# Kernel tuning notes

Measured on AMD Instinct MI355X. Metric: run time of the kernel, lower is better.

Reference implementation:

```python
import jax, jax.numpy as jnp
import numpy as np

CURVS = (-1.0, 0.0, 1.0, -0.5)
N, E, B = 50000, 800000, 128
IN, HID, OUT, GHID = 128, 128, 128, 32
K = len(CURVS)
TAU_MIN, TAU_MAX = 0.05, 10.0
EPS = 1e-15


def _vnorm(x):
    return jnp.maximum(jnp.linalg.norm(x, axis=-1, keepdims=True), EPS)


def tan_k(x, k):
    if k > 0:
        sk = np.sqrt(k)
        return jnp.tan(x * sk) / sk
    if k < 0:
        sk = np.sqrt(-k)
        return jnp.tanh(x * sk) / sk
    return x


def artan_k(x, k):
    if k > 0:
        sk = np.sqrt(k)
        return jnp.arctan(x * sk) / sk
    if k < 0:
        sk = np.sqrt(-k)
        return jnp.arctanh(jnp.clip(x * sk, -1.0 + 1e-7, 1.0 - 1e-7)) / sk
    return x


def project(x, k):
    # clip inside Poincare ball for k<0; identity otherwise (geoopt Stereographic.projx)
    if k < 0:
        maxn = (1.0 - 1e-5) / np.sqrt(-k)
        n = _vnorm(x)
        return jnp.where(n > maxn, x * (maxn / n), x)
    return x


def expmap0(u, k):
    n = _vnorm(u)
    return project(tan_k(n, k) * u / n, k)


def logmap0(y, k):
    n = _vnorm(y)
    return artan_k(n, k) * y / n


def mobius_add(x, y, k):
    x2 = jnp.sum(x * x, -1, keepdims=True)
    y2 = jnp.sum(y * y, -1, keepdims=True)
    xy = jnp.sum(x * y, -1, keepdims=True)
    num = (1.0 - 2.0 * k * xy - k * y2) * x + (1.0 + k * x2) * y
    den = jnp.maximum(1.0 - 2.0 * k * xy + k * k * x2 * y2, 1e-15)
    return project(num / den, k)


def mobius_matvec(W, x, k):
    mx = x @ W.T
    if k == 0:
        return mx
    xn = _vnorm(x)
    mxn = _vnorm(mx)
    res = tan_k(mxn / xn * artan_k(xn, k), k) * mx / mxn
    res = jnp.where(jnp.sum(jnp.abs(mx), -1, keepdims=True) == 0.0, 0.0, res)
    return project(res, k)


def dist(x, y, k):
    return 2.0 * artan_k(_vnorm(mobius_add(-x, y, k)), k)[..., 0]


def setup_inputs():
    key = jax.random.key(0)
    ks = jax.random.split(key, 12)
    x = jax.random.normal(ks[0], (N, IN), jnp.float32)
    edge_index = jax.random.randint(ks[1], (2, E), 0, N)
    batch = jnp.sort(jax.random.randint(ks[2], (N,), 0, B))
    s1 = float(np.sqrt(2.0 / (IN + HID)))
    s2 = float(np.sqrt(2.0 / (HID + OUT)))
    sg1 = float(np.sqrt(2.0 / (IN + GHID)))
    sg2 = float(np.sqrt(2.0 / (GHID + OUT)))
    raw0 = float(np.log(np.expm1(1.0 - TAU_MIN)))
    return {
        "x": x,
        "edge_index": edge_index,
        "batch": batch,
        "expert_w1": jax.random.normal(ks[3], (K, HID, IN), jnp.float32) * s1,
        "expert_b1": jnp.zeros((K, HID), jnp.float32),
        "expert_w2": jax.random.normal(ks[4], (K, OUT, HID), jnp.float32) * s2,
        "expert_b2": jnp.zeros((K, OUT), jnp.float32),
        "gate_w1": jax.random.normal(ks[5], (GHID, IN), jnp.float32) * sg1,
        "gate_b1": jnp.zeros((GHID,), jnp.float32),
        "gate_w2": jax.random.normal(ks[6], (OUT, GHID), jnp.float32) * sg2,
        "gate_b2": jnp.zeros((OUT,), jnp.float32),
        "gate_u": jax.random.normal(ks[7], (K, OUT), jnp.float32) * 0.02,
        "tau_raw": jnp.full((K,), raw0, jnp.float32),
    }


def _graph_norm(edge_index):
    loops = jnp.arange(N)
    row = jnp.concatenate([edge_index[0], loops])
    col = jnp.concatenate([edge_index[1], loops])
    deg = jax.ops.segment_sum(jnp.ones(E + N, jnp.float32), col, num_segments=N)
    dinv = deg ** -0.5  # deg >= 1 due to self loops
    return row, col, dinv[row] * dinv[col]


def _kappa_conv(xm, W, b, row, col, enorm, k):
    h = mobius_matvec(W, xm, k)
    bias_pt = expmap0(b[None, :], k)  # proju at origin is identity
    h = mobius_add(h, bias_pt, k)
    t = logmap0(h, k)  # [N, out]
    agg = jax.ops.segment_sum(enorm[:, None] * t[row], col, num_segments=N)
    return expmap0(agg, k)


def reference(x, edge_index, batch, expert_w1, expert_b1, expert_w2, expert_b2,
              gate_w1, gate_b1, gate_w2, gate_b2, gate_u, tau_raw):
    x = x.astype(jnp.float32)
    row, col, enorm = _graph_norm(edge_index)
    counts = jnp.maximum(
        jax.ops.segment_sum(jnp.ones(N, jnp.float32), batch, num_segments=B), 1.0)[:, None]

    # --- Riemannian experts ---
    embs = []
    for i, kv in enumerate(CURVS):
        xm = expmap0(x, kv)  # manifold init (proju at origin = identity)
        xm = _kappa_conv(xm, expert_w1[i], expert_b1[i], row, col, enorm, kv)
        xm = _kappa_conv(xm, expert_w2[i], expert_b2[i], row, col, enorm, kv)
        z = logmap0(xm, kv)
        embs.append(jax.ops.segment_sum(z, batch, num_segments=B) / counts)
    features = jnp.concatenate(embs, axis=-1)  # [B, K*OUT]

    # --- Euclidean gating encoder (GCN) ---
    def gcn(h, W, b):
        m = (h @ W.T)
        out = jax.ops.segment_sum(enorm[:, None] * m[row], col, num_segments=N) + b
        return jax.nn.relu(out)

    g = gcn(x, gate_w1, gate_b1)
    g = gcn(g, gate_w2, gate_b2)
    hgate = jax.ops.segment_sum(g, batch, num_segments=B) / counts  # [B, OUT]

    # --- Geometric distance gate ---
    tau = jnp.clip(jax.nn.softplus(tau_raw) + TAU_MIN, TAU_MIN, TAU_MAX)
    dists = []
    for i, kv in enumerate(CURVS):
        zk = expmap0(hgate, kv)
        yk = expmap0(gate_u[i][None, :], kv)
        dists.append(dist(zk, yk, kv))
    dists = jnp.stack(dists, axis=-1)  # [B, K]
    weights = jax.nn.softmax(-dists / tau[None, :], axis=-1)

    scaled = features * jnp.repeat(weights, OUT, axis=1)
    return scaled, weights, dists, tau
```

## Files before the change

kernel.cpp:

```cpp
#include <hip/hip_runtime.h>
#include <math.h>

#define NN 50000
#define EE 800000
#define ETOT (EE + NN)
#define BB 128
#define DIM 128
#define GHID 32
#define CHUNK 128
#define NCHUNK ((ETOT + CHUNK - 1) / CHUNK)
#define SCB 196

typedef _Float16 f16;
typedef _Float16 f16x2 __attribute__((ext_vector_type(2)));
typedef _Float16 f16x8 __attribute__((ext_vector_type(8)));
typedef float f32x4 __attribute__((ext_vector_type(4)));

struct CurvPack {
  float k[4], sk[4], mx[4], thr2[4];
};

__device__ __forceinline__ float wsum64(float v) {
#pragma unroll
  for (int m = 32; m; m >>= 1) v += __shfl_xor(v, m, 64);
  return v;
}

__device__ __forceinline__ float tan_k_d(float x, float kv, float sk) {
  if (kv > 0.f) return tanf(x * sk) / sk;
  if (kv < 0.f) return tanhf(x * sk) / sk;
  return x;
}

__device__ __forceinline__ float artan_k_d(float x, float kv, float sk) {
  if (kv > 0.f) return atanf(x * sk) / sk;
  if (kv < 0.f) {
    float t = x * sk;
    t = fminf(fmaxf(t, -1.f + 1e-7f), 1.f - 1e-7f);
    return atanhf(t) / sk;
  }
  return x;
}

__device__ __forceinline__ float proj_scale_d(float n, float kv, float maxn) {
  if (kv < 0.f && n > maxn) return maxn / n;
  return 1.f;
}

__global__ void k_init(float* __restrict__ deg, int n) {
  int i = blockIdx.x * 256 + threadIdx.x;
  if (i < n) deg[i] = 1.0f;
}

__global__ void k_counts(const int* __restrict__ batch, int* __restrict__ boff,
                         float* __restrict__ counts, int n) {
  int b = threadIdx.x;
  if (b <= 128) {
    int lo = 0, hi = n;
    while (lo < hi) {
      int mid = (lo + hi) >> 1;
      if (batch[mid] < b) lo = mid + 1; else hi = mid;
    }
    boff[b] = lo;
  }
  __syncthreads();
  if (b < 128) counts[b] = (float)(boff[b + 1] - boff[b]);
}

__global__ void k_deg(const int* __restrict__ ei, float* __restrict__ deg, int e) {
  int i = blockIdx.x * 256 + threadIdx.x;
  if (i < e) atomicAdd(&deg[ei[e + i]], 1.0f);
}

__global__ void k_dinv(float* __restrict__ deg, int* __restrict__ ideg, int n) {
  int i = blockIdx.x * 256 + threadIdx.x;
  if (i < n) {
    float d = deg[i];
    ideg[i] = (int)(d + 0.5f);
    deg[i] = 1.0f / sqrtf(d);
  }
}

__global__ void k_scanA(const int* __restrict__ ideg, int* __restrict__ bsum, int n) {
  __shared__ int ls[4];
  int i = blockIdx.x * 256 + threadIdx.x;
  int v = (i < n) ? ideg[i] : 0;
#pragma unroll
  for (int m = 1; m < 64; m <<= 1) v += __shfl_xor(v, m, 64);
  if ((threadIdx.x & 63) == 0) ls[threadIdx.x >> 6] = v;
  __syncthreads();
  if (threadIdx.x == 0) bsum[blockIdx.x] = ls[0] + ls[1] + ls[2] + ls[3];
}

__global__ void k_scanB(int* __restrict__ bsum, int nb) {
  __shared__ int wsh[4];
  int tid = threadIdx.x;
  int lane = tid & 63, w = tid >> 6;
  int v = (tid < nb) ? bsum[tid] : 0;
  int x = v;
#pragma unroll
  for (int o = 1; o < 64; o <<= 1) {
    int t = __shfl_up(x, o, 64);
    if (lane >= o) x += t;
  }
  if (lane == 63) wsh[w] = x;
  __syncthreads();
  int add = 0;
  for (int k2 = 0; k2 < w; k2++) add += wsh[k2];
  if (tid < nb) bsum[tid] = add + x - v;
}

__global__ void k_scanC(const int* __restrict__ ideg, const int* __restrict__ bsum,
                        int* __restrict__ off, int* __restrict__ cursor, int n) {
  __shared__ int wsh[4];
  int i = blockIdx.x * 256 + threadIdx.x;
  int lane = threadIdx.x & 63, w = threadIdx.x >> 6;
  int v = (i < n) ? ideg[i] : 0;
  int x = v;
#pragma unroll
  for (int o = 1; o < 64; o <<= 1) {
    int t = __shfl_up(x, o, 64);
    if (lane >= o) x += t;
  }
  if (lane == 63) wsh[w] = x;
  __syncthreads();
  int add = bsum[blockIdx.x];
  for (int k2 = 0; k2 < w; k2++) add += wsh[k2];
  int excl = add + x - v;
  if (i < n) {
    off[i] = excl;
    cursor[i] = excl;
  }
  if (i == n - 1) off[n] = excl + v;
}

__global__ void k_bnodes(const int* __restrict__ off, int* __restrict__ bnode, int nchunk,
                         int n) {
  int g = blockIdx.x * 256 + threadIdx.x;
  if (g >= nchunk) return;
  int e0 = g * CHUNK;
  int lo = 0, hi = n;
  while (hi - lo > 1) {
    int mid = (lo + hi) >> 1;
    if (off[mid] <= e0) lo = mid; else hi = mid;
  }
  bnode[g] = lo;
}

__global__ void k_bslot(const int* __restrict__ bnode, int* __restrict__ bslot, int nchunk) {
  int g = blockIdx.x * 256 + threadIdx.x;
  if (g >= nchunk) return;
  int v = bnode[g];
  int lo = 0, hi = g;
  while (lo < hi) {
    int mid = (lo + hi) >> 1;
    if (bnode[mid] < v) lo = mid + 1; else hi = mid;
  }
  bslot[g] = lo;
}

__device__ __forceinline__ bool span_head(const int* bnode, const int* bslot, const int* off,
                                          int g, int& nd) {
  if (bslot[g] != g) return false;
  nd = bnode[g];
  int s = off[nd], e = off[nd + 1];
  return (s / CHUNK) != ((e - 1) / CHUNK);
}

__global__ void k_zeroc(const int* __restrict__ bnode, const int* __restrict__ bslot,
                        const int* __restrict__ off, float* __restrict__ aggc, int nchunk) {
  int g = blockIdx.x * 4 + (threadIdx.x >> 6);
  int lane = threadIdx.x & 63;
  if (g >= nchunk) return;
  int nd;
  if (!span_head(bnode, bslot, off, g, nd)) return;
  float2 z = make_float2(0.f, 0.f);
#pragma unroll
  for (int i = 0; i < 5; i++) ((float2*)aggc)[(size_t)g * 320 + i * 64 + lane] = z;
}

__global__ void k_place(const int* __restrict__ ei, const float* __restrict__ dinv,
                        int* __restrict__ cursor, int2* __restrict__ esw, int e, int n) {
  int i = blockIdx.x * 256 + threadIdx.x;
  int et = e + n;
  if (i >= et) return;
  int r_, c_;
  if (i < e) {
    r_ = ei[i];
    c_ = ei[e + i];
  } else {
    r_ = i - e;
    c_ = i - e;
  }
  int p = atomicAdd(&cursor[c_], 1);
  esw[p] = make_int2(r_, __float_as_int(dinv[r_] * dinv[c_]));
}

__global__ void k_biaspt_all(const float* __restrict__ eb1, const float* __restrict__ eb2,
                             float* __restrict__ biasb, CurvPack cp) {
  __shared__ float l2[2];
  int blk = blockIdx.x;
  int ex = blk >> 1, layer = blk & 1;
  float kv = cp.k[ex], sk = cp.sk[ex], maxn = cp.mx[ex];
  const float* b = (layer ? eb2 : eb1) + ex * 128;
  float* outb = biasb + blk * 132;
  int j = threadIdx.x;
  float v = b[j];
  float n2 = wsum64(v * v);
  if ((j & 63) == 0) l2[j >> 6] = n2;
  __syncthreads();
  n2 = l2[0] + l2[1];
  float nraw = sqrtf(n2);
  float nnv = fmaxf(nraw, 1e-15f);
  float tk = tan_k_d(nnv, kv, sk);
  float s = tk / nnv;
  float pn = fmaxf(fabsf(tk) * (nraw / nnv), 1e-15f);
  float ps = proj_scale_d(pn, kv, maxn);
  float bp = ps * s * v;
  outb[j] = bp;
  float y2v = wsum64(bp * bp);
  __syncthreads();
  if ((j & 63) == 0) l2[j >> 6] = y2v;
  __syncthreads();
  if (j == 0) outb[128] = l2[0] + l2[1];
}

__global__ void k_w2h(const float* __restrict__ ew1, const float* __restrict__ ew2,
                      f16* __restrict__ whi, f16* __restrict__ wlo) {
  int i = blockIdx.x * 256 + threadIdx.x;
  if (i >= 8 * 16384) return;
  int slot = i >> 14;
  int r = i & 16383;
  int ex = slot >> 1, layer = slot & 1;
  float w = (layer ? ew2 : ew1)[ex * 16384 + r];
  f16 h = (f16)w;
  whi[i] = h;
  wlo[i] = (f16)(w - (float)h);
}

__global__ __launch_bounds__(256) void k_matmfma(
    const float* __restrict__ A, int astr, int aoffPerEx,
    const f16* __restrict__ whiB, const f16* __restrict__ wloB,
    const float* __restrict__ biasB, int layer, f16* __restrict__ tout, int n,
    CurvPack cp) {
  __shared__ float red[3][16][4];
  __shared__ float redT[16][4];
  __shared__ float nAs[16], nCs[16], nL[16];
  int ex = blockIdx.y;
  float kv = cp.k[ex], sk = cp.sk[ex], maxn = cp.mx[ex];
  const f16* whi = whiB + (size_t)(ex * 2 + layer) * 16384;
  const f16* wlo = wloB + (size_t)(ex * 2 + layer) * 16384;
  const float* biasb = biasB + (ex * 2 + layer) * 132;

  int tid = threadIdx.x;
  int w = tid >> 6;
  int lane = tid & 63;
  int col = lane & 15;
  int quad = lane >> 4;
  int n0w = blockIdx.x * 16;
  if (n0w >= n) return;

  int anodec = min(n0w + col, n - 1);
  const float* arow = A + (size_t)anodec * astr + ex * aoffPerEx;
  int jt0 = w * 2;

  f32x4 acc[2];
  acc[0] = (f32x4){0.f, 0.f, 0.f, 0.f};
  acc[1] = (f32x4){0.f, 0.f, 0.f, 0.f};
  float a_n2 = 0.f;

#pragma unroll
  for (int kc = 0; kc < 4; kc++) {
    int kb = kc * 32 + quad * 8;
    float4 a0 = *(const float4*)(arow + kb);
    float4 a1 = *(const float4*)(arow + kb + 4);
    float av[8] = {a0.x, a0.y, a0.z, a0.w, a1.x, a1.y, a1.z, a1.w};
    f16x8 Ah, Al;
#pragma unroll
    for (int i = 0; i < 8; i++) {
      a_n2 = fmaf(av[i], av[i], a_n2);
      f16 h = (f16)av[i];
      Ah[i] = h;
      Al[i] = (f16)(av[i] - (float)h);
    }
#pragma unroll
    for (int j2 = 0; j2 < 2; j2++) {
      const f16* bh = whi + (size_t)((jt0 + j2) * 16 + col) * 128 + kb;
      const f16* bl = wlo + (size_t)((jt0 + j2) * 16 + col) * 128 + kb;
      f16x8 Bh = *(const f16x8*)bh;
      f16x8 Bl = *(const f16x8*)bl;
      acc[j2] = __builtin_amdgcn_mfma_f32_16x16x32_f16(Ah, Bh, acc[j2], 0, 0, 0);
      acc[j2] = __builtin_amdgcn_mfma_f32_16x16x32_f16(Ah, Bl, acc[j2], 0, 0, 0);
      acc[j2] = __builtin_amdgcn_mfma_f32_16x16x32_f16(Al, Bh, acc[j2], 0, 0, 0);
    }
  }
  a_n2 += __shfl_xor(a_n2, 16, 64);
  a_n2 += __shfl_xor(a_n2, 32, 64);

  float bpj[2];
  bpj[0] = biasb[jt0 * 16 + col];
  bpj[1] = biasb[(jt0 + 1) * 16 + col];
  float y2 = biasb[128];

#pragma unroll
  for (int r = 0; r < 4; r++) {
    float s0 = 0.f, s1 = 0.f, s2 = 0.f;
#pragma unroll
    for (int j2 = 0; j2 < 2; j2++) {
      float v = acc[j2][r];
      s0 = fmaf(v, v, s0);
      s1 += fabsf(v);
      s2 = fmaf(v, bpj[j2], s2);
    }
#pragma unroll
    for (int m = 1; m < 16; m <<= 1) {
      s0 += __shfl_xor(s0, m, 64);
      s1 += __shfl_xor(s1, m, 64);
      s2 += __shfl_xor(s2, m, 64);
    }
    if (col == 0) {
      red[0][quad * 4 + r][w] = s0;
      red[1][quad * 4 + r][w] = s1;
      red[2][quad * 4 + r][w] = s2;
    }
  }
  __syncthreads();

  if (tid < 16) {
    float nraw0 = sqrtf(a_n2);
    float nnv0 = fmaxf(nraw0, 1e-15f);
    float tk0 = tan_k_d(nnv0, kv, sk);
    float pn0 = fmaxf(fabsf(tk0) * (nraw0 / nnv0), 1e-15f);
    float ps0 = proj_scale_d(pn0, kv, maxn);
    float sc = (tk0 / nnv0) * ps0;
    float xnr = pn0 * ps0;

    float s0f = (red[0][tid][0] + red[0][tid][1] + red[0][tid][2] + red[0][tid][3]) * sc * sc;
    float s1f = (red[1][tid][0] + red[1][tid][1] + red[1][tid][2] + red[1][tid][3]) * fabsf(sc);
    float s2f = (red[2][tid][0] + red[2][tid][1] + red[2][tid][2] + red[2][tid][3]) * sc;
    float xn = fmaxf(xnr, 1e-15f);
    float mxraw = sqrtf(s0f);
    float mxv = fmaxf(mxraw, 1e-15f);
    float ar = artan_k_d(xn, kv, sk);
    float c1 = tan_k_d(mxv / xn * ar, kv, sk);
    float s = (s1f == 0.f) ? 0.f : c1 / mxv;
    float pn = fmaxf(fabsf(c1) * (mxraw / mxv), 1e-15f);
    float ps = (s1f == 0.f) ? 1.f : proj_scale_d(pn, kv, maxn);
    s *= ps;
    float x2 = (s * s) * s0f;
    float xy = s * s2f;
    float Aa = 1.f - 2.f * kv * xy - kv * y2;
    float Cc = 1.f + kv * x2;
    float den = fmaxf(1.f - 2.f * kv * xy + (kv * kv) * x2 * y2, 1e-15f);
    nAs[tid] = Aa * s / den * sc;
    nCs[tid] = Cc / den;
  }
  __syncthreads();

#pragma unroll
  for (int r = 0; r < 4; r++) {
    int idx = quad * 4 + r;
    float Asc = nAs[idx], Cs = nCs[idx];
    float t0 = 0.f;
#pragma unroll
    for (int j2 = 0; j2 < 2; j2++) {
      float v = fmaf(Asc, acc[j2][r], Cs * bpj[j2]);
      t0 = fmaf(v, v, t0);
    }
#pragma unroll
    for (int m = 1; m < 16; m <<= 1) t0 += __shfl_xor(t0, m, 64);
    if (col == 0) redT[idx][w] = t0;
  }
  __syncthreads();

  if (tid < 16) {
    float t0f = redT[tid][0] + redT[tid][1] + redT[tid][2] + redT[tid][3];
    float nraw = sqrtf(t0f);
    float ps2 = proj_scale_d(fmaxf(nraw, 1e-15f), kv, maxn);
    float nh = fmaxf(ps2 * nraw, 1e-15f);
    nL[tid] = artan_k_d(nh, kv, sk) / nh * ps2;
  }
  __syncthreads();

#pragma unroll
  for (int r = 0; r < 4; r++) {
    int idx = quad * 4 + r;
    int gnode = n0w + idx;
    if (gnode >= n) continue;
    float Asc = nAs[idx], Cs = nCs[idx], L = nL[idx];
    f16* trow = tout + (size_t)gnode * 512;
#pragma unroll
    for (int j2 = 0; j2 < 2; j2++) {
      float v = fmaf(Asc, acc[j2][r], Cs * bpj[j2]);
      int d = (jt0 + j2) * 16 + col;
      trow[(d >> 1) * 8 + ex * 2 + (d & 1)] = (f16)(L * v);
    }
  }
}

template <int MODE>
__global__ __launch_bounds__(256) void k_aggF(
    const int2* __restrict__ esw, const int* __restrict__ off,
    const int* __restrict__ bnode, const int* __restrict__ bslot,
    const int* __restrict__ batch, const f16x8* __restrict__ t,
    const float* __restrict__ gm1, const f16x2* __restrict__ tg,
    float* __restrict__ agg1, float* __restrict__ aggc,
    float* __restrict__ g1, float* __restrict__ feats,
    const float* __restrict__ gbias, float* __restrict__ hgate,
    int etot, CurvPack cp) {
  int gw = blockIdx.x * 4 + (threadIdx.x >> 6);
  int lane = threadIdx.x & 63;
  int e0 = gw * CHUNK;
  if (e0 >= etot) return;
  int e1 = min(e0 + CHUNK, etot);
  int bnHead = bnode[gw];
  int slotA = bslot[gw];
  int slotB = ((gw + 1) * CHUNK < etot) ? bslot[gw + 1] : slotA;
  int cur = bnHead;
  int runStart = off[cur];
  int eend = off[cur + 1];
  float ax[4], ay[4], pax[4], pay[4];
#pragma unroll
  for (int e = 0; e < 4; e++) ax[e] = ay[e] = pax[e] = pay[e] = 0.f;
  float gx = 0.f, gy = 0.f, pgx = 0.f, pgy = 0.f;
  int bcur = (MODE == 1) ? batch[cur] : 0;
  float bbx, bby = 0.f;
  if (MODE == 0) {
    bbx = gbias[lane & 31];
  } else {
    float2 bb = ((const float2*)gbias)[lane];
    bbx = bb.x;
    bby = bb.y;
  }

  auto flushInterior = [&]() {
#pragma unroll
    for (int e = 0; e < 4; e++) {
      if (MODE == 0) {
        ((float2*)agg1)[(size_t)cur * 256 + e * 64 + lane] = make_float2(ax[e], ay[e]);
      } else {
        float n2 = wsum64(fmaf(ax[e], ax[e], ay[e] * ay[e]));
        if (n2 <= cp.thr2[e]) {
          pax[e] += ax[e];
          pay[e] += ay[e];
        } else {
          float nraw = sqrtf(n2);
          float nnv = fmaxf(nraw, 1e-15f);
          float tk = tan_k_d(nnv, cp.k[e], cp.sk[e]);
          float s = tk / nnv;
          float pn = fmaxf(fabsf(tk) * (nraw / nnv), 1e-15f);
          float ps = proj_scale_d(pn, cp.k[e], cp.mx[e]);
          s *= ps;
          float nh = fmaxf(pn * ps, 1e-15f);
          float sc = artan_k_d(nh, cp.k[e], cp.sk[e]) / nh * s;
          pax[e] = fmaf(sc, ax[e], pax[e]);
          pay[e] = fmaf(sc, ay[e], pay[e]);
        }
      }
    }
    if (MODE == 0) {
      if (lane < 32) g1[(size_t)cur * 32 + lane] = fmaxf(gx + bbx, 0.f);
    } else {
      pgx += fmaxf(gx + bbx, 0.f);
      pgy += fmaxf(gy + bby, 0.f);
    }
  };
  auto flushBoundary = [&]() {
    int slot = (cur == bnHead) ? slotA : slotB;
    float* dp = aggc + (size_t)slot * 640;
#pragma unroll
    for (int e = 0; e < 4; e++) {
      atomicAdd(dp + e * 128 + lane * 2, ax[e]);
      atomicAdd(dp + e * 128 + lane * 2 + 1, ay[e]);
    }
    if (MODE == 0) {
      if (lane < 32) atomicAdd(dp + 512 + lane, gx);
    } else {
      atomicAdd(dp + 512 + lane * 2, gx);
      atomicAdd(dp + 512 + lane * 2 + 1, gy);
    }
  };
  auto flushPool = [&]() {
#pragma unroll
    for (int e = 0; e < 4; e++) {
      float* fp = &feats[(size_t)bcur * 512 + e * 128 + lane * 2];
      atomicAdd(fp, pax[e]);
      atomicAdd(fp + 1, pay[e]);
    }
    float* hp = &hgate[(size_t)bcur * 128 + lane * 2];
    atomicAdd(hp, pgx);
    atomicAdd(hp + 1, pgy);
  };

  for (int j = e0; j < e1; j += 8) {
    int2 mv = esw[j + (lane & 7)];
    f16x8 rv[8];
    float gvf[8];
    f16x2 gvh[8];
#pragma unroll
    for (int q = 0; q < 8; q++) {
      int s = __builtin_amdgcn_readlane(mv.x, q);
      rv[q] = t[(size_t)s * 64 + lane];
      if (MODE == 0) gvf[q] = gm1[(size_t)s * 32 + (lane & 31)];
      else gvh[q] = tg[(size_t)s * 64 + lane];
    }
#pragma unroll
    for (int q = 0; q < 8; q++) {
      if (j + q == eend) {
        if (runStart >= e0) flushInterior(); else flushBoundary();
#pragma unroll
        for (int e = 0; e < 4; e++) ax[e] = ay[e] = 0.f;
        gx = gy = 0.f;
        runStart = j + q;
        cur++;
        eend = off[cur + 1];
        if (MODE == 1) {
          int nbt = batch[cur];
          if (nbt != bcur) {
            flushPool();
#pragma unroll
            for (int e = 0; e < 4; e++) pax[e] = pay[e] = 0.f;
            pgx = pgy = 0.f;
            bcur = nbt;
          }
        }
      }
      float w = __int_as_float(__builtin_amdgcn_readlane(mv.y, q));
#pragma unroll
      for (int e = 0; e < 4; e++) {
        ax[e] = fmaf(w, (float)rv[q][2 * e], ax[e]);
        ay[e] = fmaf(w, (float)rv[q][2 * e + 1], ay[e]);
      }
      if (MODE == 0) {
        gx = fmaf(w, gvf[q], gx);
      } else {
        gx = fmaf(w, (float)gvh[q][0], gx);
        gy = fmaf(w, (float)gvh[q][1], gy);
      }
    }
  }
  if (runStart >= e0 && eend <= e1) flushInterior(); else flushBoundary();
  if (MODE == 1) flushPool();
}

__global__ void k_fix1(const int* __restrict__ bnode, const int* __restrict__ bslot,
                       const int* __restrict__ off, const float* __restrict__ aggc,
                       float* __restrict__ agg1, float* __restrict__ g1,
                       const float* __restrict__ gb1, int nchunk) {
  int g = blockIdx.x * 4 + (threadIdx.x >> 6);
  int lane = threadIdx.x & 63;
  if (g >= nchunk) return;
  int nd;
  if (!span_head(bnode, bslot, off, g, nd)) return;
  const float* sp = aggc + (size_t)g * 640;
#pragma unroll
  for (int e = 0; e < 4; e++) {
    float2 v = ((const float2*)sp)[e * 64 + lane];
    ((float2*)agg1)[(size_t)nd * 256 + e * 64 + lane] = v;
  }
  if (lane < 32) g1[(size_t)nd * 32 + lane] = fmaxf(sp[512 + lane] + gb1[lane], 0.f);
}

__global__ void k_fix2(const int* __restrict__ bnode, const int* __restrict__ bslot,
                       const int* __restrict__ off, const float* __restrict__ aggc,
                       const int* __restrict__ batch, float* __restrict__ feats,
                       const float* __restrict__ gb2, float* __restrict__ hgate,
                       int nchunk, CurvPack cp) {
  int g = blockIdx.x * 4 + (threadIdx.x >> 6);
  int lane = threadIdx.x & 63;
  if (g >= nchunk) return;
  int nd;
  if (!span_head(bnode, bslot, off, g, nd)) return;
  int b = batch[nd];
  const float* sp = aggc + (size_t)g * 640;
#pragma unroll
  for (int e = 0; e < 4; e++) {
    float2 v = ((const float2*)sp)[e * 64 + lane];
    float n2 = wsum64(fmaf(v.x, v.x, v.y * v.y));
    float nraw = sqrtf(n2);
    float nnv = fmaxf(nraw, 1e-15f);
    float tk = tan_k_d(nnv, cp.k[e], cp.sk[e]);
    float s = tk / nnv;
    float pn = fmaxf(fabsf(tk) * (nraw / nnv), 1e-15f);
    float ps = proj_scale_d(pn, cp.k[e], cp.mx[e]);
    s *= ps;
    float nh = fmaxf(pn * ps, 1e-15f);
    float sc = artan_k_d(nh, cp.k[e], cp.sk[e]) / nh * s;
    float* fp = &feats[(size_t)b * 512 + e * 128 + lane * 2];
    atomicAdd(fp, sc * v.x);
    atomicAdd(fp + 1, sc * v.y);
  }
  float2 gv = ((const float2*)(sp + 512))[lane];
  float2 bb = ((const float2*)gb2)[lane];
  float* hp = &hgate[(size_t)b * 128 + lane * 2];
  atomicAdd(hp, fmaxf(gv.x + bb.x, 0.f));
  atomicAdd(hp + 1, fmaxf(gv.y + bb.y, 0.f));
}

__global__ __launch_bounds__(256) void k_gate1(const float* __restrict__ x,
                                               const float* __restrict__ gw1,
                                               float* __restrict__ m1, int n) {
  __shared__ float xT[64][68];
  __shared__ float Wt[64][36];
  int tid = threadIdx.x;
  int n0 = blockIdx.x * 64;
  int c = tid & 7, r = tid >> 3;
  float acc[2][4];
#pragma unroll
  for (int i = 0; i < 2; i++)
#pragma unroll
    for (int jj = 0; jj < 4; jj++) acc[i][jj] = 0.f;

  for (int kc = 0; kc < 2; kc++) {
    if (kc) __syncthreads();
#pragma unroll
    for (int it = 0; it < 8; it++) {
      int u = tid + it * 256;
      int j = u >> 6, kd = u & 63;
      Wt[kd][j] = gw1[j * 128 + kc * 64 + kd];
    }
#pragma unroll
    for (int it = 0; it < 4; it++) {
      int u = tid + it * 256;
      int node = u >> 4, c4 = u & 15;
      float4 v = make_float4(0.f, 0.f, 0.f, 0.f);
      if (n0 + node < n) v = ((const float4*)x)[(size_t)(n0 + node) * 32 + kc * 16 + c4];
      xT[4 * c4 + 0][node] = v.x;
      xT[4 * c4 + 1][node] = v.y;
      xT[4 * c4 + 2][node] = v.z;
      xT[4 * c4 + 3][node] = v.w;
    }
    __syncthreads();
#pragma unroll 8
    for (int kd = 0; kd < 64; kd++) {
      float2 av = *(const float2*)&xT[kd][r * 2];
      float4 bv = *(const float4*)&Wt[kd][c * 4];
      float a[2] = {av.x, av.y};
      float bbv[4] = {bv.x, bv.y, bv.z, bv.w};
#pragma unroll
      for (int i = 0; i < 2; i++)
#pragma unroll
        for (int jj = 0; jj < 4; jj++) acc[i][jj] = fmaf(a[i], bbv[jj], acc[i][jj]);
    }
  }
#pragma unroll
  for (int i = 0; i < 2; i++) {
    int node = n0 + r * 2 + i;
    if (node >= n) continue;
    ((float4*)m1)[(size_t)node * 8 + c] = make_float4(acc[i][0], acc[i][1], acc[i][2], acc[i][3]);
  }
}

__global__ __launch_bounds__(256) void k_gate2(const float* __restrict__ g1,
                                               const float* __restrict__ gw2,
                                               f16* __restrict__ m2, int n) {
  __shared__ float xT[32][68];
  __shared__ float Wt[32][132];
  int tid = threadIdx.x;
  int n0 = blockIdx.x * 64;
  int c = tid & 15, r = tid >> 4;
  float acc[4][8];
#pragma unroll
  for (int i = 0; i < 4; i++)
#pragma unroll
    for (int jj = 0; jj < 8; jj++) acc[i][jj] = 0.f;

#pragma unroll
  for (int it = 0; it < 16; it++) {
    int u = tid + it * 256;
    int j = u >> 5, kd = u & 31;
    Wt[kd][j] = gw2[j * 32 + kd];
  }
#pragma unroll
  for (int it = 0; it < 2; it++) {
    int u = tid + it * 256;
    int node = u >> 3, c4 = u & 7;
    float4 v = make_float4(0.f, 0.f, 0.f, 0.f);
    if (n0 + node < n) v = ((const float4*)g1)[(size_t)(n0 + node) * 8 + c4];
    xT[4 * c4 + 0][node] = v.x;
    xT[4 * c4 + 1][node] = v.y;
    xT[4 * c4 + 2][node] = v.z;
    xT[4 * c4 + 3][node] = v.w;
  }
  __syncthreads();
#pragma unroll 8
  for (int kd = 0; kd < 32; kd++) {
    float4 av = *(const float4*)&xT[kd][r * 4];
    float4 b0 = *(const float4*)&Wt[kd][c * 8];
    float4 b1 = *(const float4*)&Wt[kd][c * 8 + 4];
    float a[4] = {av.x, av.y, av.z, av.w};
    float bbv[8] = {b0.x, b0.y, b0.z, b0.w, b1.x, b1.y, b1.z, b1.w};
#pragma unroll
    for (int i = 0; i < 4; i++)
#pragma unroll
      for (int jj = 0; jj < 8; jj++) acc[i][jj] = fmaf(a[i], bbv[jj], acc[i][jj]);
  }
#pragma unroll
  for (int i = 0; i < 4; i++) {
    int node = n0 + r * 4 + i;
    if (node >= n) continue;
    f16x8 hv;
#pragma unroll
    for (int jj = 0; jj < 8; jj++) hv[jj] = (f16)acc[i][jj];
    *((f16x8*)(m2 + (size_t)node * 128) + c) = hv;
  }
}

__global__ __launch_bounds__(128) void k_final(const float* __restrict__ feats,
                                               const float* __restrict__ hgate,
                                               const float* __restrict__ counts,
                                               const float* __restrict__ gate_u,
                                               const float* __restrict__ tau_raw,
                                               float* __restrict__ out, CurvPack cp) {
  __shared__ float l2[2];
  int b = blockIdx.x;
  int j = threadIdx.x;
  float cnt = fmaxf(counts[b], 1.f);
  float hg = hgate[(size_t)b * 128 + j] / cnt;

  auto bsum = [&](float v) -> float {
    v = wsum64(v);
    __syncthreads();
    if ((j & 63) == 0) l2[j >> 6] = v;
    __syncthreads();
    return l2[0] + l2[1];
  };

  float nhg2 = bsum(hg * hg);
  float nhgraw = sqrtf(nhg2);
  float nhg = fmaxf(nhgraw, 1e-15f);

  float d[4], tau[4];
#pragma unroll
  for (int i = 0; i < 4; i++) {
    float kv = cp.k[i], sk = cp.sk[i], mxn = cp.mx[i];
    float tk = tan_k_d(nhg, kv, sk);
    float s = tk / nhg;
    float pn = fmaxf(fabsf(tk) * (nhgraw / nhg), 1e-15f);
    s *= proj_scale_d(pn, kv, mxn);
    float zk = s * hg;

    float u = gate_u[i * 128 + j];
    float nu2 = bsum(u * u);
    float nuraw = sqrtf(nu2);
    float nu = fmaxf(nuraw, 1e-15f);
    float tku = tan_k_d(nu, kv, sk);
    float su = tku / nu;
    float pnu = fmaxf(fabsf(tku) * (nuraw / nu), 1e-15f);
    su *= proj_scale_d(pnu, kv, mxn);
    float yk = su * u;

    float xv = -zk;
    float x2 = bsum(xv * xv);
    float y2 = bsum(yk * yk);
    float xy = bsum(xv * yk);
    float A = 1.f - 2.f * kv * xy - kv * y2;
    float C = 1.f + kv * x2;
    float den = fmaxf(1.f - 2.f * kv * xy + (kv * kv) * x2 * y2, 1e-15f);
    float ma = (A * xv + C * yk) / den;
    float m2 = bsum(ma * ma);
    float mraw = sqrtf(m2);
    float ps2 = proj_scale_d(fmaxf(mraw, 1e-15f), kv, mxn);
    float nm = fmaxf(ps2 * mraw, 1e-15f);
    d[i] = 2.f * artan_k_d(nm, kv, sk);

    float tr = tau_raw[i];
    tau[i] = fminf(fmaxf(log1pf(expf(tr)) + 0.05f, 0.05f), 10.f);
  }

  float xi[4];
  float mxv = -1e30f;
#pragma unroll
  for (int i = 0; i < 4; i++) {
    xi[i] = -d[i] / tau[i];
    mxv = fmaxf(mxv, xi[i]);
  }
  float es = 0.f, e[4];
#pragma unroll
  for (int i = 0; i < 4; i++) {
    e[i] = expf(xi[i] - mxv);
    es += e[i];
  }
  float w[4];
#pragma unroll
  for (int i = 0; i < 4; i++) w[i] = e[i] / es;

#pragma unroll
  for (int i = 0; i < 4; i++)
    out[(size_t)b * 512 + i * 128 + j] = feats[(size_t)b * 512 + i * 128 + j] / cnt * w[i];

  if (j < 4) {
    out[65536 + b * 4 + j] = w[j];
    out[66048 + b * 4 + j] = d[j];
  }
  if (b == 0 && j < 4) out[66560 + j] = tau[j];
}

extern "C" void kernel_launch(void* const* d_in, const int* in_sizes, int n_in,
                              void* d_out, int out_size, void* d_ws, size_t ws_size,
                              hipStream_t stream) {
  const float* x = (const float*)d_in[0];
  const int* ei = (const int*)d_in[1];
  const int* batch = (const int*)d_in[2];
  const float* ew1 = (const float*)d_in[3];
  const float* eb1 = (const float*)d_in[4];
  const float* ew2 = (const float*)d_in[5];
  const float* eb2 = (const float*)d_in[6];
  const float* gw1 = (const float*)d_in[7];
  const float* gb1 = (const float*)d_in[8];
  const float* gw2 = (const float*)d_in[9];
  const float* gb2 = (const float*)d_in[10];
  const float* gu = (const float*)d_in[11];
  const float* traw = (const float*)d_in[12];
  float* out = (float*)d_out;

  const int N = NN, E = EE, ET = ETOT, B = BB;

  float* ws = (float*)d_ws;
  size_t o = 0;
  f16* t4 = (f16*)ws;       o += (size_t)N * 256;
  float* agg1 = ws + o;     o += (size_t)N * 512;
  float* aggc = ws + o;     o += (size_t)NCHUNK * 640;
  float* deg = ws + o;      o += N;
  float* counts = ws + o;   o += 256;
  float* feats = ws + o;    o += (size_t)B * 512;
  float* hg = ws + o;       o += (size_t)B * 128;
  float* biasb = ws + o;    o += 8 * 132;
  f16* whi = (f16*)(ws + o);    o += 8 * 16384 / 2;
  f16* wlo = (f16*)(ws + o);    o += 8 * 16384 / 2;
  float* m1 = ws + o;       o += (size_t)N * 32;
  float* g1 = ws + o;       o += (size_t)N * 32;
  f16* tg = (f16*)(ws + o); o += (size_t)N * 64;
  int* ideg = (int*)(ws + o);   o += N;
  int* csroff = (int*)(ws + o); o += N + 8;
  int* cursor = (int*)(ws + o); o += N;
  int* boff = (int*)(ws + o);   o += 136;
  int* bsum = (int*)(ws + o);   o += 256;
  int* bnode = (int*)(ws + o);  o += NCHUNK + 8;
  int* bslot = (int*)(ws + o);  o += NCHUNK + 8;
  int2* esw = (int2*)(ws + o);  o += (size_t)2 * ET;

  hipMemsetAsync(counts, 0, (256 + (size_t)B * 512 + (size_t)B * 128) * sizeof(float), stream);

  const double curvs[4] = {-1.0, 0.0, 1.0, -0.5};
  CurvPack cp;
  for (int i = 0; i < 4; i++) {
    double kd = curvs[i];
    double skd = sqrt(fabs(kd));
    cp.k[i] = (float)kd;
    cp.sk[i] = (float)skd;
    cp.mx[i] = (kd < 0) ? (float)((1.0 - 1e-5) / skd) : 3.0e38f;
    if (kd < 0) {
      double thr = 6.0 / skd;
      cp.thr2[i] = (float)(thr * thr);
    } else if (kd > 0) {
      double thr = 1.5 / skd;
      cp.thr2[i] = (float)(thr * thr);
    } else {
      cp.thr2[i] = 3.0e38f;
    }
  }

  k_init<<<(N + 255) / 256, 256, 0, stream>>>(deg, N);
  k_counts<<<1, 256, 0, stream>>>(batch, boff, counts, N);
  k_deg<<<(E + 255) / 256, 256, 0, stream>>>(ei, deg, E);
  k_dinv<<<(N + 255) / 256, 256, 0, stream>>>(deg, ideg, N);
  k_scanA<<<SCB, 256, 0, stream>>>(ideg, bsum, N);
  k_scanB<<<1, 256, 0, stream>>>(bsum, SCB);
  k_scanC<<<SCB, 256, 0, stream>>>(ideg, bsum, csroff, cursor, N);
  k_bnodes<<<(NCHUNK + 255) / 256, 256, 0, stream>>>(csroff, bnode, NCHUNK, N);
  k_bslot<<<(NCHUNK + 255) / 256, 256, 0, stream>>>(bnode, bslot, NCHUNK);
  k_place<<<(ET + 255) / 256, 256, 0, stream>>>(ei, deg, cursor, esw, E, N);
  k_biaspt_all<<<8, 128, 0, stream>>>(eb1, eb2, biasb, cp);
  k_w2h<<<512, 256, 0, stream>>>(ew1, ew2, whi, wlo);
  k_gate1<<<(N + 63) / 64, 256, 0, stream>>>(x, gw1, m1, N);

  const int aggBlocks = (NCHUNK + 3) / 4;
  dim3 mfmaGrid((N + 15) / 16, 4);

  k_matmfma<<<mfmaGrid, 256, 0, stream>>>(x, 128, 0, whi, wlo, biasb, 0, t4, N, cp);
  k_zeroc<<<aggBlocks, 256, 0, stream>>>(bnode, bslot, csroff, aggc, NCHUNK);
  k_aggF<0><<<aggBlocks, 256, 0, stream>>>(esw, csroff, bnode, bslot, batch,
                                           (const f16x8*)t4, m1, nullptr, agg1, aggc, g1,
                                           nullptr, gb1, nullptr, ET, cp);
  k_fix1<<<aggBlocks, 256, 0, stream>>>(bnode, bslot, csroff, aggc, agg1, g1, gb1, NCHUNK);
  k_gate2<<<(N + 63) / 64, 256, 0, stream>>>(g1, gw2, tg, N);

  k_matmfma<<<mfmaGrid, 256, 0, stream>>>(agg1, 512, 128, whi, wlo, biasb, 1, t4, N, cp);
  k_zeroc<<<aggBlocks, 256, 0, stream>>>(bnode, bslot, csroff, aggc, NCHUNK);
  k_aggF<1><<<aggBlocks, 256, 0, stream>>>(esw, csroff, bnode, bslot, batch,
                                           (const f16x8*)t4, nullptr, (const f16x2*)tg,
                                           nullptr, aggc, nullptr, feats, gb2, hg, ET, cp);
  k_fix2<<<aggBlocks, 256, 0, stream>>>(bnode, bslot, csroff, aggc, batch, feats, gb2, hg,
                                        NCHUNK, cp);

  k_final<<<B, 128, 0, stream>>>(feats, hg, counts, gu, traw, out, cp);

  (void)in_sizes; (void)n_in; (void)out_size; (void)ws_size;
}
```

Before: 960.1 us.

## Double-buffer edge gather loads in aggregation kernel and halve edge chunk size

Restructures the edge aggregation loop in k_aggF to prefetch the next block of eight source-row gathers (two register buffers) while the current block is accumulated, so gather latency overlaps with the FMA work. Edge-metadata loads are clamped to stay in bounds. The edge chunk per wavefront drops from 128 to 64, which gives more wavefronts and better load balance but more boundary flushes and atomics. The extra buffers raise register use, which may lower occupancy.

After: 1.071 ms. 11.5% more time.

```diff
diff --git a/kernel.cpp b/kernel.cpp
--- a/kernel.cpp
+++ b/kernel.cpp
@@ -7,7 +7,7 @@
 #define BB 128
 #define DIM 128
 #define GHID 32
-#define CHUNK 128
+#define CHUNK 64
 #define NCHUNK ((ETOT + CHUNK - 1) / CHUNK)
 #define SCB 196
 
@@ -413,6 +413,8 @@
   int e0 = gw * CHUNK;
   if (e0 >= etot) return;
   int e1 = min(e0 + CHUNK, etot);
+  int lane7 = lane & 7;
+  int lane31 = lane & 31;
   int bnHead = bnode[gw];
   int slotA = bslot[gw];
   int slotB = ((gw + 1) * CHUNK < etot) ? bslot[gw + 1] : slotA;
@@ -426,7 +428,7 @@
   int bcur = (MODE == 1) ? batch[cur] : 0;
   float bbx, bby = 0.f;
   if (MODE == 0) {
-    bbx = gbias[lane & 31];
+    bbx = gbias[lane31];
   } else {
     float2 bb = ((const float2*)gbias)[lane];
     bbx = bb.x;
@@ -492,55 +494,80 @@
     atomicAdd(hp + 1, pgy);
   };
 
-  for (int j = e0; j < e1; j += 8) {
-    int2 mv = esw[j + (lane & 7)];
-    f16x8 rv[8];
-    float gvf[8];
-    f16x2 gvh[8];
-#pragma unroll
-    for (int q = 0; q < 8; q++) {
-      int s = __builtin_amdgcn_readlane(mv.x, q);
-      rv[q] = t[(size_t)s * 64 + lane];
-      if (MODE == 0) gvf[q] = gm1[(size_t)s * 32 + (lane & 31)];
-      else gvh[q] = tg[(size_t)s * 64 + lane];
-    }
-#pragma unroll
-    for (int q = 0; q < 8; q++) {
-      if (j + q == eend) {
-        if (runStart >= e0) flushInterior(); else flushBoundary();
-#pragma unroll
-        for (int e = 0; e < 4; e++) ax[e] = ay[e] = 0.f;
-        gx = gy = 0.f;
-        runStart = j + q;
-        cur++;
-        eend = off[cur + 1];
-        if (MODE == 1) {
-          int nbt = batch[cur];
-          if (nbt != bcur) {
-            flushPool();
-#pragma unroll
-            for (int e = 0; e < 4; e++) pax[e] = pay[e] = 0.f;
-            pgx = pgy = 0.f;
-            bcur = nbt;
-          }
-        }
-      }
-      float w = __int_as_float(__builtin_amdgcn_readlane(mv.y, q));
-#pragma unroll
-      for (int e = 0; e < 4; e++) {
-        ax[e] = fmaf(w, (float)rv[q][2 * e], ax[e]);
-        ay[e] = fmaf(w, (float)rv[q][2 * e + 1], ay[e]);
-      }
-      if (MODE == 0) {
-        gx = fmaf(w, gvf[q], gx);
-      } else {
-        gx = fmaf(w, (float)gvh[q][0], gx);
-        gy = fmaf(w, (float)gvh[q][1], gy);
-      }
-    }
+  f16x8 rvA[8], rvB[8];
+  float gfA[8], gfB[8];
+  f16x2 ghA[8], ghB[8];
+
+#define LOADM(JJ) esw[min((JJ) + lane7, etot - 1)]
+
+#define ISSUE8(RV, GF, GH, MV)                                        \
+  {                                                                   \
+    _Pragma("unroll") for (int q = 0; q < 8; q++) {                   \
+      int s = __builtin_amdgcn_readlane((MV).x, q);                   \
+      RV[q] = t[(size_t)s * 64 + lane];                               \
+      if (MODE == 0) GF[q] = gm1[(size_t)s * 32 + lane31];            \
+      else GH[q] = tg[(size_t)s * 64 + lane];                         \
+    }                                                                 \
+  }
+
+#define PROCESS8(RV, GF, GH, MV, JB)                                  \
+  {                                                                   \
+    _Pragma("unroll") for (int q = 0; q < 8; q++) {                   \
+      if ((JB) + q == eend) {                                         \
+        if (runStart >= e0) flushInterior(); else flushBoundary();    \
+        _Pragma("unroll") for (int e = 0; e < 4; e++) ax[e] = ay[e] = 0.f; \
+        gx = gy = 0.f;                                                \
+        runStart = (JB) + q;                                          \
+        cur++;                                                        \
+        eend = off[cur + 1];                                          \
+        if (MODE == 1) {                                              \
+          int nbt = batch[cur];                                       \
+          if (nbt != bcur) {                                          \
+            flushPool();                                              \
+            _Pragma("unroll") for (int e = 0; e < 4; e++) pax[e] = pay[e] = 0.f; \
+            pgx = pgy = 0.f;                                          \
+            bcur = nbt;                                               \
+          }                                                           \
+        }                                                             \
+      }                                                               \
+      float w = __int_as_float(__builtin_amdgcn_readlane((MV).y, q)); \
+      _Pragma("unroll") for (int e = 0; e < 4; e++) {                 \
+        ax[e] = fmaf(w, (float)RV[q][2 * e], ax[e]);                  \
+        ay[e] = fmaf(w, (float)RV[q][2 * e + 1], ay[e]);              \
+      }                                                               \
+      if (MODE == 0) {                                                \
+        gx = fmaf(w, GF[q], gx);                                      \
+      } else {                                                        \
+        gx = fmaf(w, (float)GH[q][0], gx);                            \
+        gy = fmaf(w, (float)GH[q][1], gy);                            \
+      }                                                               \
+    }                                                                 \
+  }
+
+  int nb = (e1 - e0) >> 3;
+  int2 mvA = LOADM(e0);
+  int2 mvB = LOADM(e0 + 8);
+  ISSUE8(rvA, gfA, ghA, mvA);
+
+  int j = e0;
+  for (int b = 0; b < nb; b += 2, j += 16) {
+    int2 mvC = LOADM(j + 16);
+    ISSUE8(rvB, gfB, ghB, mvB);
+    PROCESS8(rvA, gfA, ghA, mvA, j);
+    int2 mvD = LOADM(j + 24);
+    if (b + 2 < nb) {
+      ISSUE8(rvA, gfA, ghA, mvC);
+    }
+    PROCESS8(rvB, gfB, ghB, mvB, j + 8);
+    mvA = mvC;
+    mvB = mvD;
   }
   if (runStart >= e0 && eend <= e1) flushInterior(); else flushBoundary();
   if (MODE == 1) flushPool();
+
+#undef LOADM
+#undef ISSUE8
+#undef PROCESS8
 }
 
 __global__ void k_fix1(const int* __restrict__ bnode, const int* __restrict__ bslot,
```

## Halve edge chunk size and preload all chunk edge metadata in one load

Applied to the files above, without the earlier changes.

Halves the per-wavefront edge chunk from 128 to 64, which doubles the number of wavefronts over the edge list and gives more parallelism and better load balance in the aggregation kernel. Each lane now loads one (src, weight) pair for the whole chunk up front, and the gather loop is fully unrolled with readlane, so the per-group-of-8 metadata load drops out of the loop. The cost is more chunk-boundary fixups and atomics, plus possible register pressure from the unroll.

After: 1.069 ms. +11.3%, slower.

```diff
diff --git a/kernel.cpp b/kernel.cpp
--- a/kernel.cpp
+++ b/kernel.cpp
@@ -7,7 +7,7 @@
 #define BB 128
 #define DIM 128
 #define GHID 32
-#define CHUNK 128
+#define CHUNK 64
 #define NCHUNK ((ETOT + CHUNK - 1) / CHUNK)
 #define SCB 196
 
@@ -413,12 +413,16 @@
   int e0 = gw * CHUNK;
   if (e0 >= etot) return;
   int e1 = min(e0 + CHUNK, etot);
+  int lane31 = lane & 31;
   int bnHead = bnode[gw];
   int slotA = bslot[gw];
   int slotB = ((gw + 1) * CHUNK < etot) ? bslot[gw + 1] : slotA;
   int cur = bnHead;
   int runStart = off[cur];
   int eend = off[cur + 1];
+
+  int2 mv = esw[min(e0 + lane, etot - 1)];
+
   float ax[4], ay[4], pax[4], pay[4];
 #pragma unroll
   for (int e = 0; e < 4; e++) ax[e] = ay[e] = pax[e] = pay[e] = 0.f;
@@ -426,7 +430,7 @@
   int bcur = (MODE == 1) ? batch[cur] : 0;
   float bbx, bby = 0.f;
   if (MODE == 0) {
-    bbx = gbias[lane & 31];
+    bbx = gbias[lane31];
   } else {
     float2 bb = ((const float2*)gbias)[lane];
     bbx = bb.x;
@@ -492,50 +496,54 @@
     atomicAdd(hp + 1, pgy);
   };
 
-  for (int j = e0; j < e1; j += 8) {
-    int2 mv = esw[j + (lane & 7)];
-    f16x8 rv[8];
-    float gvf[8];
-    f16x2 gvh[8];
-#pragma unroll
-    for (int q = 0; q < 8; q++) {
-      int s = __builtin_amdgcn_readlane(mv.x, q);
-      rv[q] = t[(size_t)s * 64 + lane];
-      if (MODE == 0) gvf[q] = gm1[(size_t)s * 32 + (lane & 31)];
-      else gvh[q] = tg[(size_t)s * 64 + lane];
-    }
-#pragma unroll
-    for (int q = 0; q < 8; q++) {
-      if (j + q == eend) {
-        if (runStart >= e0) flushInterior(); else flushBoundary();
-#pragma unroll
-        for (int e = 0; e < 4; e++) ax[e] = ay[e] = 0.f;
-        gx = gy = 0.f;
-        runStart = j + q;
-        cur++;
-        eend = off[cur + 1];
-        if (MODE == 1) {
-          int nbt = batch[cur];
-          if (nbt != bcur) {
-            flushPool();
-#pragma unroll
-            for (int e = 0; e < 4; e++) pax[e] = pay[e] = 0.f;
-            pgx = pgy = 0.f;
-            bcur = nbt;
+  f16x8 rv[8];
+  float gf[8];
+  f16x2 gh[8];
+
+#pragma unroll
+  for (int b = 0; b < CHUNK / 8; b++) {
+    int jb = e0 + b * 8;
+    if (jb < e1) {
+#pragma unroll
+      for (int q = 0; q < 8; q++) {
+        int s = __builtin_amdgcn_readlane(mv.x, b * 8 + q);
+        rv[q] = t[(size_t)s * 64 + lane];
+        if (MODE == 0) gf[q] = gm1[(size_t)s * 32 + lane31];
+        else gh[q] = tg[(size_t)s * 64 + lane];
+      }
+#pragma unroll
+      for (int q = 0; q < 8; q++) {
+        if (jb + q == eend) {
+          if (runStart >= e0) flushInterior(); else flushBoundary();
+#pragma unroll
+          for (int e = 0; e < 4; e++) ax[e] = ay[e] = 0.f;
+          gx = gy = 0.f;
+          runStart = jb + q;
+          cur++;
+          eend = off[cur + 1];
+          if (MODE == 1) {
+            int nbt = batch[cur];
+            if (nbt != bcur) {
+              flushPool();
+#pragma unroll
+              for (int e = 0; e < 4; e++) pax[e] = pay[e] = 0.f;
+              pgx = pgy = 0.f;
+              bcur = nbt;
+            }
           }
         }
-      }
-      float w = __int_as_float(__builtin_amdgcn_readlane(mv.y, q));
-#pragma unroll
-      for (int e = 0; e < 4; e++) {
-        ax[e] = fmaf(w, (float)rv[q][2 * e], ax[e]);
-        ay[e] = fmaf(w, (float)rv[q][2 * e + 1], ay[e]);
-      }
-      if (MODE == 0) {
-        gx = fmaf(w, gvf[q], gx);
-      } else {
-        gx = fmaf(w, (float)gvh[q][0], gx);
-        gy = fmaf(w, (float)gvh[q][1], gy);
+        float w = __int_as_float(__builtin_amdgcn_readlane(mv.y, b * 8 + q));
+#pragma unroll
+        for (int e = 0; e < 4; e++) {
+          ax[e] = fmaf(w, (float)rv[q][2 * e], ax[e]);
+          ay[e] = fmaf(w, (float)rv[q][2 * e + 1], ay[e]);
+        }
+        if (MODE == 0) {
+          gx = fmaf(w, gf[q], gx);
+        } else {
+          gx = fmaf(w, (float)gh[q][0], gx);
+          gy = fmaf(w, (float)gh[q][1], gy);
+        }
       }
     }
   }
```
